# Performance work log

Measured on AMD Instinct MI355X. Metric: run time of the kernel, lower is better.

Reference implementation:

```python
import jax, jax.numpy as jnp
import numpy as np

OBS = jnp.array([0, 3, 6, 9, 12])
LO, HI = 0.001, 2.0

def gamma(x):
    return LO + (HI - LO) * jax.nn.sigmoid(x)

def full_chain_rhs(y, k):
    # y: (B,13) species, k: (B,19) rate constants
    A, B_, C, D, E, F, G, H, I, J, K_, L, M = [y[..., i] for i in range(13)]
    (kf1, kf2, kf3, kf4, kf5, kf6, kf7, kf8, kf9, kf10, kf11, kf12,
     kr1, kr3, kr5, kr7, kr9, kr11, kr12) = [k[..., i] for i in range(19)]
    dA = -kf1 * A + kr1 * B_
    dB = kf1 * A - kr1 * B_ - kf2 * B_
    dC = kf2 * B_ - kf3 * C + kr3 * D
    dD = kf3 * C - kr3 * D - kf4 * D
    dE = kf4 * D - kf5 * E + kr5 * F
    dF = kf5 * E - kr5 * F - kf6 * F
    dG = kf6 * F - kf7 * G + kr7 * H
    dH = kf7 * G - kr7 * H - kf8 * H
    dI = kf8 * H - kf9 * I + kr9 * J
    dJ = kf9 * I - kr9 * J - kf10 * J
    dK = kf10 * J - kf11 * K_ + kr11 * L
    dL = kf11 * K_ - kr11 * L - kf12 * L + kr12 * M
    dM = kf12 * L - kr12 * M
    return jnp.stack([dA, dB, dC, dD, dE, dF, dG, dH, dI, dJ, dK, dL, dM], axis=-1)

def rk4_step(y, dt, k):
    # y:(B,13) dt:(B,1) k:(B,19)
    k1 = full_chain_rhs(y, k)
    k2 = full_chain_rhs(y + 0.5 * dt * k1, k)
    k3 = full_chain_rhs(y + 0.5 * dt * k2, k)
    k4 = full_chain_rhs(y + dt * k3, k)
    return jnp.maximum(y + dt / 6.0 * (k1 + 2.0 * k2 + 2.0 * k3 + k4), 0.0)

def setup_inputs() -> dict:
    B, K, U, P = 2048, 256, 4, 5
    LIFT, HID = 32, 128
    key = jax.random.key(0)
    ks = jax.random.split(key, 9)
    in_dim = U + P
    def xavier(k, shape):
        lim = np.sqrt(6.0 / (shape[0] + shape[1])).astype(np.float32)
        return jax.random.uniform(k, shape, jnp.float32, -lim, lim)
    return {
        "y0": jax.random.uniform(ks[0], (B, P), jnp.float32),
        "u_seq": jax.random.normal(ks[1], (B, K, U), jnp.float32) * 0.1,
        "dt_seq": jax.random.uniform(ks[2], (B, K), jnp.float32, 0.01, 0.1),
        "y_seq": jax.random.uniform(ks[3], (B, K, P), jnp.float32),
        "W_lift": xavier(ks[4], (in_dim, LIFT)),
        "b_lift": jnp.zeros((LIFT,), jnp.float32),
        "w_ih": xavier(ks[5], (3 * HID, LIFT)),
        "w_hh": xavier(ks[6], (3 * HID, HID)),
        "b_ih": jnp.zeros((3 * HID,), jnp.float32),
        "b_hh": jnp.zeros((3 * HID,), jnp.float32),
        "W_head": xavier(ks[7], (HID, 19)),
        "b_head": jnp.zeros((19,), jnp.float32),
        "u_to_y_jump": jax.random.normal(ks[8], (U, P), jnp.float32) * 0.05,
        "tf_every": 50,
    }

def reference(y0, u_seq, dt_seq, y_seq, W_lift, b_lift, w_ih, w_hh, b_ih, b_hh, W_head, b_head, u_to_y_jump, tf_every):
    B, K, _ = u_seq.shape
    HID = w_hh.shape[1]
    # init hidden full state: 0.01 everywhere, obs slots get y0 + 0.01
    y_full0 = jnp.full((B, 13), 0.01, u_seq.dtype).at[:, OBS].set(y0 + 0.01)
    h0 = jnp.zeros((B, HID), u_seq.dtype)
    t = jnp.arange(K)
    tf_mask = (t > 0) & (t % tf_every == 0)  # teacher-forcing steps
    y_seq_prev = jnp.concatenate([jnp.zeros_like(y_seq[:, :1]), y_seq[:, :-1]], axis=1)
    xs = (jnp.swapaxes(u_seq, 0, 1), dt_seq.T[..., None],
          jnp.swapaxes(y_seq_prev, 0, 1), tf_mask)

    def step(carry, x):
        y_full, h = carry
        u_k, dt_k, y_prev_tf, m = x
        y_obs_prev = y_full[:, OBS]
        y_prev_in = jax.lax.stop_gradient(jnp.where(m, y_prev_tf, y_obs_prev))
        feat = jnp.concatenate([u_k, y_prev_in], axis=-1)
        lifted = jax.nn.silu(feat @ W_lift + b_lift)
        # PyTorch GRU cell
        gx = lifted @ w_ih.T + b_ih
        gh = h @ w_hh.T + b_hh
        rx, zx, nx = jnp.split(gx, 3, axis=-1)
        rh, zh, nh = jnp.split(gh, 3, axis=-1)
        r = jax.nn.sigmoid(rx + rh)
        z = jax.nn.sigmoid(zx + zh)
        n = jnp.tanh(nx + r * nh)
        h_new = (1.0 - z) * n + z * h
        theta = gamma(h_new @ W_head + b_head)  # (B,19), all bounds (0.001,2.0)
        y_obs_jump = y_obs_prev + u_k @ u_to_y_jump
        y_full_jump = y_full.at[:, OBS].set(y_obs_jump)
        y_full_next = rk4_step(y_full_jump, dt_k, theta)  # n_sub=1 as in forward
        return (y_full_next, h_new), (y_full_next[:, OBS], theta)

    _, (y_out, theta_out) = jax.lax.scan(step, (y_full0, h0), xs)
    return jnp.swapaxes(y_out, 0, 1), jnp.swapaxes(theta_out, 0, 1)
```

## Files before the change

kernel.cpp:

```cpp
#include <hip/hip_runtime.h>
#include <cstddef>
#include <cstdint>

#define NB 8
#define NTHREADS 640
#define HID 128
#define LIFT 32
#define NSP 13
#define NTH 19

typedef __attribute__((ext_vector_type(8))) short short8;
typedef __attribute__((ext_vector_type(4))) float f32x4;

__device__ const int c_kidx[13][4] = {
  {0,12,0,0},{0,12,1,0},{1,2,13,0},{2,13,3,0},{3,4,14,0},{4,14,5,0},
  {5,6,15,0},{6,15,7,0},{7,8,16,0},{8,16,9,0},{9,10,17,0},{10,17,11,18},{11,18,0,0}
};
__device__ const int c_yidx[13][4] = {
  {0,1,0,0},{0,1,1,0},{1,2,3,0},{2,3,3,0},{3,4,5,0},{4,5,5,0},
  {5,6,7,0},{6,7,7,0},{7,8,9,0},{8,9,9,0},{9,10,11,0},{10,11,11,12},{11,12,0,0}
};
__device__ const float c_sgn[13][4] = {
  {-1.f, 1.f, 0.f, 0.f},{ 1.f,-1.f,-1.f, 0.f},{ 1.f,-1.f, 1.f, 0.f},
  { 1.f,-1.f,-1.f, 0.f},{ 1.f,-1.f, 1.f, 0.f},{ 1.f,-1.f,-1.f, 0.f},
  { 1.f,-1.f, 1.f, 0.f},{ 1.f,-1.f,-1.f, 0.f},{ 1.f,-1.f, 1.f, 0.f},
  { 1.f,-1.f,-1.f, 0.f},{ 1.f,-1.f, 1.f, 0.f},{ 1.f,-1.f,-1.f, 1.f},
  { 1.f,-1.f, 0.f, 0.f}
};

__device__ __forceinline__ uint32_t pk(float a, float b) {
  uint32_t ua = __float_as_uint(a), ub = __float_as_uint(b);
  ua = (ua + 0x7FFFu + ((ua >> 16) & 1u)) >> 16;
  ub = (ub + 0x7FFFu + ((ub >> 16) & 1u)) >> 16;
  return ua | (ub << 16);
}
__device__ __forceinline__ float sigm(float a) { return 1.f/(1.f + __expf(-a)); }

union FragU { uint4 u; short8 s; };
__device__ __forceinline__ short8 ldfrag(const float* p) {
  FragU t;
  const float4 a = *reinterpret_cast<const float4*>(p);
  const float4 b = *reinterpret_cast<const float4*>(p+4);
  t.u = make_uint4(pk(a.x,a.y), pk(a.z,a.w), pk(b.x,b.y), pk(b.z,b.w));
  return t.s;
}

struct Smem {
  uint32_t whF[8*3*4*64*4];
  uint32_t whdF[2*4*64*4];
  uint32_t hF[4*64*4];
  uint32_t liftF[64*4];
  float theta[8*20];
};

__global__ __launch_bounds__(NTHREADS)
void fullmodel_rnn(const float* __restrict__ y0,
                   const float* __restrict__ u_seq,
                   const float* __restrict__ dt_seq,
                   const float* __restrict__ y_seq,
                   const float* __restrict__ W_lift,
                   const float* __restrict__ b_lift,
                   const float* __restrict__ w_ih,
                   const float* __restrict__ w_hh,
                   const float* __restrict__ b_ih,
                   const float* __restrict__ b_hh,
                   const float* __restrict__ W_head,
                   const float* __restrict__ b_head,
                   const float* __restrict__ u2y,
                   const int*  __restrict__ tf_every_p,
                   float* __restrict__ out,
                   int K, int theta_off)
{
  extern __shared__ __align__(16) char smem_raw[];
  Smem& S = *reinterpret_cast<Smem*>(smem_raw);

  const int tid  = threadIdx.x;
  const int wid  = tid >> 6;
  const int lane = tid & 63;
  const int q    = lane >> 4;
  const int col  = lane & 15;
  const int bg0  = blockIdx.x * NB;
  const int tf_every = tf_every_p[0];
  const bool gatew = (wid < 8);

  for (int f = tid; f < 8*3*4*64; f += NTHREADS) {
    int l = f & 63, idx = f >> 6;
    int s = idx & 3; idx >>= 2;
    int g = idx % 3, w = idx / 3;
    int row = 128*g + 16*w + (l & 15);
    int k0 = 32*s + 8*(l >> 4);
    const float* p = w_hh + (size_t)row*HID + k0;
    uint32_t* d = S.whF + (size_t)f*4;
    d[0]=pk(p[0],p[1]); d[1]=pk(p[2],p[3]); d[2]=pk(p[4],p[5]); d[3]=pk(p[6],p[7]);
  }
  for (int f = tid; f < 2*4*64; f += NTHREADS) {
    int l = f & 63, idx = f >> 6;
    int s = idx & 3, T = idx >> 2;
    int o = 16*T + (l & 15);
    int k0 = 32*s + 8*(l >> 4);
    uint32_t* d = S.whdF + (size_t)f*4;
    if (o < NTH) {
#pragma unroll
      for (int c=0;c<4;++c)
        d[c] = pk(W_head[(size_t)(k0+2*c)*NTH + o], W_head[(size_t)(k0+2*c+1)*NTH + o]);
    } else {
#pragma unroll
      for (int c=0;c<4;++c) d[c] = 0u;
    }
  }
  for (int f = tid; f < 4*64*4; f += NTHREADS) S.hF[f] = 0u;
  for (int f = tid; f < 64*4;   f += NTHREADS) S.liftF[f] = 0u;

  const uint32_t* hf_p  = &S.hF[lane*4];
  const uint32_t* lf_p  = &S.liftF[lane*4];
  const uint32_t* whp   = S.whF + ((size_t)wid*12*64 + lane)*4;
  const uint32_t* whdp  = S.whdF + (size_t)lane*4;

  float bsumR[4], bsumZ[4], bihn_[4], bhhn_[4], h_old[4];
  short8 wir, wiz, win;
  if (gatew) {
    const int rowR = 16*wid + col, kq = 8*q;
    wir = ldfrag(w_ih + (size_t)rowR*LIFT + kq);
    wiz = ldfrag(w_ih + (size_t)(128+rowR)*LIFT + kq);
    win = ldfrag(w_ih + (size_t)(256+rowR)*LIFT + kq);
#pragma unroll
    for (int r2=0;r2<4;++r2) {
      const int i0 = 16*wid + 4*q + r2;
      bsumR[r2] = b_ih[i0]     + b_hh[i0];
      bsumZ[r2] = b_ih[128+i0] + b_hh[128+i0];
      bihn_[r2] = b_ih[256+i0];
      bhhn_[r2] = b_hh[256+i0];
      h_old[r2] = 0.f;
    }
  }

  float bhd[2][4] = {{0,0,0,0},{0,0,0,0}};
  float wa0=0,wa1=0,wa2=0,wa3=0,wa4=0,wa5=0,wa6=0,wa7=0,wa8=0;
  float wb0=0,wb1=0,wb2=0,wb3=0,wb4=0,wb5=0,wb6=0,wb7=0,wb8=0;
  float blA=0.f, blB=0.f;
  const int base_b = (wid == 9) ? 4 : 0;
  const int b_loc = lane / NSP, rs = lane - NSP*b_loc;
  const bool rk_lane = (!gatew) && (lane < 52);
  const int bl8 = base_b + b_loc;
  const int gb = bg0 + (rk_lane ? bl8 : 0);
  const bool obs = rk_lane && (rs % 3 == 0);
  const int ro = rs / 3;
  float y_reg=0.f, u_cur=0.f, f_src=0.f;
  float sg_[4]={0,0,0,0}, u2yv[4]={0,0,0,0};
  int ksrc[4]={0,0,0,0}, ysrc[4]={0,0,0,0};
  float* outT0 = out; float* outY = out;
  if (!gatew) {
#pragma unroll
    for (int T=0;T<2;++T)
#pragma unroll
      for (int r2=0;r2<4;++r2) {
        const int o = 16*T + 4*q + r2;
        bhd[T][r2] = (o < NTH) ? b_head[o] : 0.f;
      }
    const int li = 2*col;
    wa0=W_lift[0*32+li]; wa1=W_lift[1*32+li]; wa2=W_lift[2*32+li];
    wa3=W_lift[3*32+li]; wa4=W_lift[4*32+li]; wa5=W_lift[5*32+li];
    wa6=W_lift[6*32+li]; wa7=W_lift[7*32+li]; wa8=W_lift[8*32+li];
    wb0=W_lift[0*32+li+1]; wb1=W_lift[1*32+li+1]; wb2=W_lift[2*32+li+1];
    wb3=W_lift[3*32+li+1]; wb4=W_lift[4*32+li+1]; wb5=W_lift[5*32+li+1];
    wb6=W_lift[6*32+li+1]; wb7=W_lift[7*32+li+1]; wb8=W_lift[8*32+li+1];
    blA = b_lift[li]; blB = b_lift[li+1];
    outT0 = out + (size_t)theta_off + ((size_t)(bg0+col))*K*NTH + 4*q;
    __builtin_amdgcn_s_setprio(2);
  }
  if (rk_lane) {
#pragma unroll
    for (int j=0;j<4;++j) { sg_[j]=c_sgn[rs][j]; ksrc[j]=c_kidx[rs][j]; ysrc[j]=NSP*b_loc + c_yidx[rs][j]; }
    y_reg = 0.01f + (obs ? y0[gb*5 + ro] : 0.f);
    if (rs < 4) u_cur = u_seq[(size_t)gb*K*4 + rs];
    if (obs) { for (int d=0;d<4;++d) u2yv[d] = u2y[d*5 + ro]; }
    f_src = y_reg;
    outY = out + ((size_t)gb*K)*5 + ro;
  }
  __syncthreads();

  for (int k = 0; k <= K; ++k) {
    f32x4 accR={0,0,0,0}, accZ={0,0,0,0}, accNH={0,0,0,0};

    if (gatew) {
      if (k < K) {
        FragU h0,h1,h2,h3;
        h0.u = *reinterpret_cast<const uint4*>(hf_p);
        h1.u = *reinterpret_cast<const uint4*>(hf_p + 256);
        h2.u = *reinterpret_cast<const uint4*>(hf_p + 512);
        h3.u = *reinterpret_cast<const uint4*>(hf_p + 768);
#pragma unroll
        for (int ss=0; ss<4; ++ss) {
          FragU ar,az,an;
          ar.u = *reinterpret_cast<const uint4*>(whp + (0*4+ss)*256);
          az.u = *reinterpret_cast<const uint4*>(whp + (1*4+ss)*256);
          an.u = *reinterpret_cast<const uint4*>(whp + (2*4+ss)*256);
          const short8 hb = (ss==0)?h0.s:(ss==1)?h1.s:(ss==2)?h2.s:h3.s;
          accR  = __builtin_amdgcn_mfma_f32_16x16x32_bf16(ar.s, hb, accR, 0,0,0);
          accZ  = __builtin_amdgcn_mfma_f32_16x16x32_bf16(az.s, hb, accZ, 0,0,0);
          accNH = __builtin_amdgcn_mfma_f32_16x16x32_bf16(an.s, hb, accNH, 0,0,0);
        }
      }
    } else {
      const int s = k - 1;
      float dt_v=0.f, u_nxt=0.f, ysq_v=0.f;
      if (rk_lane) {
        if (k >= 1) {
          if (rs == 4) dt_v  = dt_seq[(size_t)gb*K + s];
          if (obs)     ysq_v = y_seq[((size_t)gb*K + s)*5 + ro];
        }
        if (k < K && rs < 4) u_nxt = u_seq[((size_t)gb*K + k)*4 + rs];
      }
      if (k >= 1) {
        f32x4 at0={0,0,0,0}, at1={0,0,0,0};
        FragU h0,h1,h2,h3;
        h0.u = *reinterpret_cast<const uint4*>(hf_p);
        h1.u = *reinterpret_cast<const uint4*>(hf_p + 256);
        h2.u = *reinterpret_cast<const uint4*>(hf_p + 512);
        h3.u = *reinterpret_cast<const uint4*>(hf_p + 768);
#pragma unroll
        for (int ss=0; ss<4; ++ss) {
          FragU a0,a1;
          a0.u = *reinterpret_cast<const uint4*>(whdp + (0*4+ss)*256);
          a1.u = *reinterpret_cast<const uint4*>(whdp + (1*4+ss)*256);
          const short8 hb = (ss==0)?h0.s:(ss==1)?h1.s:(ss==2)?h2.s:h3.s;
          at0 = __builtin_amdgcn_mfma_f32_16x16x32_bf16(a0.s, hb, at0, 0,0,0);
          at1 = __builtin_amdgcn_mfma_f32_16x16x32_bf16(a1.s, hb, at1, 0,0,0);
        }
        if (col >= base_b && col < base_b + 4) {
          f32x4 th0;
#pragma unroll
          for (int r2=0;r2<4;++r2) th0[r2] = 0.001f + 1.999f*sigm(at0[r2] + bhd[0][r2]);
          *reinterpret_cast<f32x4*>(&S.theta[col*20 + 4*q]) = th0;
          outT0[0]=th0[0]; outT0[1]=th0[1]; outT0[2]=th0[2]; outT0[3]=th0[3];
          if (q == 0) {
            f32x4 th1;
#pragma unroll
            for (int r2=0;r2<4;++r2) th1[r2] = 0.001f + 1.999f*sigm(at1[r2] + bhd[1][r2]);
            *reinterpret_cast<f32x4*>(&S.theta[col*20 + 16]) = th1;
            outT0[16]=th1[0]; outT0[17]=th1[1]; outT0[18]=th1[2];
          }
        }
        if (rk_lane) {
          const float dtv = __shfl(dt_v, NSP*b_loc + 4);
          const float u0 = __shfl(u_cur, NSP*b_loc + 0);
          const float u1 = __shfl(u_cur, NSP*b_loc + 1);
          const float u2 = __shfl(u_cur, NSP*b_loc + 2);
          const float u3 = __shfl(u_cur, NSP*b_loc + 3);
          const float q0 = sg_[0]*S.theta[bl8*20 + ksrc[0]];
          const float q1 = sg_[1]*S.theta[bl8*20 + ksrc[1]];
          const float q2 = sg_[2]*S.theta[bl8*20 + ksrc[2]];
          const float q3 = sg_[3]*S.theta[bl8*20 + ksrc[3]];
          float yj = y_reg;
          if (obs) yj += u0*u2yv[0] + u1*u2yv[1] + u2*u2yv[2] + u3*u2yv[3];
          float yc = yj;
          const float k1 = q0*__shfl(yc,ysrc[0]) + q1*__shfl(yc,ysrc[1]) + q2*__shfl(yc,ysrc[2]) + q3*__shfl(yc,ysrc[3]);
          yc = fmaf(0.5f*dtv, k1, yj);
          const float k2 = q0*__shfl(yc,ysrc[0]) + q1*__shfl(yc,ysrc[1]) + q2*__shfl(yc,ysrc[2]) + q3*__shfl(yc,ysrc[3]);
          yc = fmaf(0.5f*dtv, k2, yj);
          const float k3 = q0*__shfl(yc,ysrc[0]) + q1*__shfl(yc,ysrc[1]) + q2*__shfl(yc,ysrc[2]) + q3*__shfl(yc,ysrc[3]);
          yc = fmaf(dtv, k3, yj);
          const float k4 = q0*__shfl(yc,ysrc[0]) + q1*__shfl(yc,ysrc[1]) + q2*__shfl(yc,ysrc[2]) + q3*__shfl(yc,ysrc[3]);
          const float yn = fmaxf(fmaf(dtv*(1.f/6.f), k1 + 2.f*k2 + 2.f*k3 + k4, yj), 0.f);
          y_reg = yn;
          if (obs) *outY = yn;
          if (k < K) {
            const bool m_next = (k % tf_every) == 0;
            u_cur = u_nxt;
            if (obs) f_src = m_next ? ysq_v : yn;
          }
        }
        outT0 += NTH; outY += 5;
      }
      if (k < K) {
        const int g4 = NSP*(lane >> 4);
        const float fu0 = __shfl(u_cur, g4+0), fu1 = __shfl(u_cur, g4+1);
        const float fu2 = __shfl(u_cur, g4+2), fu3 = __shfl(u_cur, g4+3);
        const float fy0 = __shfl(f_src, g4+0), fy1 = __shfl(f_src, g4+3);
        const float fy2 = __shfl(f_src, g4+6), fy3 = __shfl(f_src, g4+9);
        const float fy4 = __shfl(f_src, g4+12);
        float a = blA + fu0*wa0 + fu1*wa1 + fu2*wa2 + fu3*wa3
                      + fy0*wa4 + fy1*wa5 + fy2*wa6 + fy3*wa7 + fy4*wa8;
        float b = blB + fu0*wb0 + fu1*wb1 + fu2*wb2 + fu3*wb3
                      + fy0*wb4 + fy1*wb5 + fy2*wb6 + fy3*wb7 + fy4*wb8;
        const float va = a*sigm(a), vb = b*sigm(b);
        const int bL = base_b + (lane >> 4);
        S.liftF[(col>>2)*64 + bL*4 + (col&3)] = pk(va, vb);
      }
    }
    __syncthreads();

    if (gatew && k < K) {
      FragU lf; lf.u = *reinterpret_cast<const uint4*>(lf_p);
      accR = __builtin_amdgcn_mfma_f32_16x16x32_bf16(wir, lf.s, accR, 0,0,0);
      accZ = __builtin_amdgcn_mfma_f32_16x16x32_bf16(wiz, lf.s, accZ, 0,0,0);
      f32x4 z4 = {0,0,0,0};
      f32x4 accNX = __builtin_amdgcn_mfma_f32_16x16x32_bf16(win, lf.s, z4, 0,0,0);
      float hn[4];
#pragma unroll
      for (int r2=0;r2<4;++r2) {
        const float rg = sigm(accR[r2] + bsumR[r2]);
        const float zg = sigm(accZ[r2] + bsumZ[r2]);
        const float nx = accNX[r2] + bihn_[r2];
        const float nh = accNH[r2] + bhhn_[r2];
        const float e  = __expf(2.f*(nx + rg*nh));
        const float ng = 1.f - 2.f/(e + 1.f);
        hn[r2] = (1.f - zg)*ng + zg*h_old[r2];
        h_old[r2] = hn[r2];
      }
      const int word = (wid>>1)*256 + ((((2*wid)+(q>>1))&3)*16 + col)*4 + 2*(q&1);
      *reinterpret_cast<uint2*>(&S.hF[word]) = make_uint2(pk(hn[0],hn[1]), pk(hn[2],hn[3]));
    }
    __syncthreads();
  }
}

extern "C" void kernel_launch(void* const* d_in, const int* in_sizes, int n_in,
                              void* d_out, int out_size, void* d_ws, size_t ws_size,
                              hipStream_t stream) {
  const float* y0     = (const float*)d_in[0];
  const float* u_seq  = (const float*)d_in[1];
  const float* dt_seq = (const float*)d_in[2];
  const float* y_seq  = (const float*)d_in[3];
  const float* W_lift = (const float*)d_in[4];
  const float* b_lift = (const float*)d_in[5];
  const float* w_ih   = (const float*)d_in[6];
  const float* w_hh   = (const float*)d_in[7];
  const float* b_ih   = (const float*)d_in[8];
  const float* b_hh   = (const float*)d_in[9];
  const float* W_head = (const float*)d_in[10];
  const float* b_head = (const float*)d_in[11];
  const float* u2y    = (const float*)d_in[12];
  const int*   tfe    = (const int*)d_in[13];
  float* out = (float*)d_out;

  const int B = in_sizes[0] / 5;
  const int K = in_sizes[2] / B;
  const int theta_off = B * K * 5;

  (void)hipFuncSetAttribute((const void*)fullmodel_rnn,
                            hipFuncAttributeMaxDynamicSharedMemorySize,
                            (int)sizeof(Smem));

  dim3 grid(B / NB), block(NTHREADS);
  hipLaunchKernelGGL(fullmodel_rnn, grid, block, sizeof(Smem), stream,
                     y0, u_seq, dt_seq, y_seq, W_lift, b_lift, w_ih, w_hh,
                     b_ih, b_hh, W_head, b_head, u2y, tfe, out, K, theta_off);
}
```

Baseline: 677.6 us.

## Keep GRU recurrent weights in registers, simplify RK4 stencil, prefetch inputs

```diff
diff --git a/kernel.cpp b/kernel.cpp
--- a/kernel.cpp
+++ b/kernel.cpp
@@ -12,21 +12,13 @@
 typedef __attribute__((ext_vector_type(8))) short short8;
 typedef __attribute__((ext_vector_type(4))) float f32x4;
 
-__device__ const int c_kidx[13][4] = {
-  {0,12,0,0},{0,12,1,0},{1,2,13,0},{2,13,3,0},{3,4,14,0},{4,14,5,0},
-  {5,6,15,0},{6,15,7,0},{7,8,16,0},{8,16,9,0},{9,10,17,0},{10,17,11,18},{11,18,0,0}
-};
-__device__ const int c_yidx[13][4] = {
-  {0,1,0,0},{0,1,1,0},{1,2,3,0},{2,3,3,0},{3,4,5,0},{4,5,5,0},
-  {5,6,7,0},{6,7,7,0},{7,8,9,0},{8,9,9,0},{9,10,11,0},{10,11,11,12},{11,12,0,0}
-};
-__device__ const float c_sgn[13][4] = {
-  {-1.f, 1.f, 0.f, 0.f},{ 1.f,-1.f,-1.f, 0.f},{ 1.f,-1.f, 1.f, 0.f},
-  { 1.f,-1.f,-1.f, 0.f},{ 1.f,-1.f, 1.f, 0.f},{ 1.f,-1.f,-1.f, 0.f},
-  { 1.f,-1.f, 1.f, 0.f},{ 1.f,-1.f,-1.f, 0.f},{ 1.f,-1.f, 1.f, 0.f},
-  { 1.f,-1.f,-1.f, 0.f},{ 1.f,-1.f, 1.f, 0.f},{ 1.f,-1.f,-1.f, 1.f},
-  { 1.f,-1.f, 0.f, 0.f}
-};
+__device__ const int   c_kA [13] = {0,0,1,2,3,4,5,6,7,8,9,10,11};
+__device__ const int   c_kB1[13] = {0,12,2,13,4,14,6,15,8,16,10,17,18};
+__device__ const int   c_kB2[13] = {0,1,0,3,0,5,0,7,0,9,0,11,0};
+__device__ const int   c_kC [13] = {12,0,13,0,14,0,15,0,16,0,17,18,0};
+__device__ const float c_mA [13] = {0.f,1.f,1.f,1.f,1.f,1.f,1.f,1.f,1.f,1.f,1.f,1.f,1.f};
+__device__ const float c_mB2[13] = {0.f,1.f,0.f,1.f,0.f,1.f,0.f,1.f,0.f,1.f,0.f,1.f,0.f};
+__device__ const float c_mC [13] = {1.f,0.f,1.f,0.f,1.f,0.f,1.f,0.f,1.f,0.f,1.f,1.f,0.f};
 
 __device__ __forceinline__ uint32_t pk(float a, float b) {
   uint32_t ua = __float_as_uint(a), ub = __float_as_uint(b);
@@ -35,6 +27,20 @@
   return ua | (ub << 16);
 }
 __device__ __forceinline__ float sigm(float a) { return 1.f/(1.f + __expf(-a)); }
+
+__device__ __forceinline__ void sync_lds() {
+  __builtin_amdgcn_sched_barrier(0);
+  asm volatile("s_waitcnt lgkmcnt(0)" ::: "memory");
+  __builtin_amdgcn_s_barrier();
+  __builtin_amdgcn_sched_barrier(0);
+}
+
+__device__ __forceinline__ float rhs3(int am1, int ap1, float cA, float cB,
+                                      float cC, float yc) {
+  const float ym1 = __int_as_float(__builtin_amdgcn_ds_bpermute(am1, __float_as_int(yc)));
+  const float yp1 = __int_as_float(__builtin_amdgcn_ds_bpermute(ap1, __float_as_int(yc)));
+  return fmaf(cA, ym1, fmaf(cB, yc, cC * yp1));
+}
 
 union FragU { uint4 u; short8 s; };
 __device__ __forceinline__ short8 ldfrag(const float* p) {
@@ -46,14 +52,13 @@
 }
 
 struct Smem {
-  uint32_t whF[8*3*4*64*4];
   uint32_t whdF[2*4*64*4];
   uint32_t hF[4*64*4];
   uint32_t liftF[64*4];
   float theta[8*20];
 };
 
-__global__ __launch_bounds__(NTHREADS)
+__global__ __launch_bounds__(NTHREADS, 3)
 void fullmodel_rnn(const float* __restrict__ y0,
                    const float* __restrict__ u_seq,
                    const float* __restrict__ dt_seq,
@@ -83,16 +88,6 @@
   const int tf_every = tf_every_p[0];
   const bool gatew = (wid < 8);
 
-  for (int f = tid; f < 8*3*4*64; f += NTHREADS) {
-    int l = f & 63, idx = f >> 6;
-    int s = idx & 3; idx >>= 2;
-    int g = idx % 3, w = idx / 3;
-    int row = 128*g + 16*w + (l & 15);
-    int k0 = 32*s + 8*(l >> 4);
-    const float* p = w_hh + (size_t)row*HID + k0;
-    uint32_t* d = S.whF + (size_t)f*4;
-    d[0]=pk(p[0],p[1]); d[1]=pk(p[2],p[3]); d[2]=pk(p[4],p[5]); d[3]=pk(p[6],p[7]);
-  }
   for (int f = tid; f < 2*4*64; f += NTHREADS) {
     int l = f & 63, idx = f >> 6;
     int s = idx & 3, T = idx >> 2;
@@ -113,16 +108,22 @@
 
   const uint32_t* hf_p  = &S.hF[lane*4];
   const uint32_t* lf_p  = &S.liftF[lane*4];
-  const uint32_t* whp   = S.whF + ((size_t)wid*12*64 + lane)*4;
   const uint32_t* whdp  = S.whdF + (size_t)lane*4;
 
   float bsumR[4], bsumZ[4], bihn_[4], bhhn_[4], h_old[4];
-  short8 wir, wiz, win;
+  short8 wfR[4], wfZ[4], wfN[4], wir, wiz, win;
   if (gatew) {
     const int rowR = 16*wid + col, kq = 8*q;
     wir = ldfrag(w_ih + (size_t)rowR*LIFT + kq);
     wiz = ldfrag(w_ih + (size_t)(128+rowR)*LIFT + kq);
     win = ldfrag(w_ih + (size_t)(256+rowR)*LIFT + kq);
+    const float* wb = w_hh + (size_t)rowR*HID + kq;
+#pragma unroll
+    for (int ss=0; ss<4; ++ss) {
+      wfR[ss] = ldfrag(wb + 32*ss);
+      wfZ[ss] = ldfrag(wb + (size_t)128*HID + 32*ss);
+      wfN[ss] = ldfrag(wb + (size_t)256*HID + 32*ss);
+    }
 #pragma unroll
     for (int r2=0;r2<4;++r2) {
       const int i0 = 16*wid + 4*q + r2;
@@ -146,8 +147,11 @@
   const bool obs = rk_lane && (rs % 3 == 0);
   const int ro = rs / 3;
   float y_reg=0.f, u_cur=0.f, f_src=0.f;
-  float sg_[4]={0,0,0,0}, u2yv[4]={0,0,0,0};
-  int ksrc[4]={0,0,0,0}, ysrc[4]={0,0,0,0};
+  float u2yv[4]={0,0,0,0};
+  int kA_=0,kB1_=0,kB2_=0,kC_=0;
+  float mA_=0.f,mB2_=0.f,mC_=0.f;
+  int am1=0, ap1=0, tfc=1;
+  float dt_c=0.f, ysq_c=0.f, u_n=0.f;
   float* outT0 = out; float* outY = out;
   if (!gatew) {
 #pragma unroll
@@ -169,15 +173,17 @@
     __builtin_amdgcn_s_setprio(2);
   }
   if (rk_lane) {
-#pragma unroll
-    for (int j=0;j<4;++j) { sg_[j]=c_sgn[rs][j]; ksrc[j]=c_kidx[rs][j]; ysrc[j]=NSP*b_loc + c_yidx[rs][j]; }
+    kA_ = c_kA[rs]; kB1_ = c_kB1[rs]; kB2_ = c_kB2[rs]; kC_ = c_kC[rs];
+    mA_ = c_mA[rs]; mB2_ = c_mB2[rs]; mC_ = c_mC[rs];
+    am1 = 4 * ((lane > 0)  ? (lane - 1) : 0);
+    ap1 = 4 * ((lane < 51) ? (lane + 1) : 51);
     y_reg = 0.01f + (obs ? y0[gb*5 + ro] : 0.f);
     if (rs < 4) u_cur = u_seq[(size_t)gb*K*4 + rs];
     if (obs) { for (int d=0;d<4;++d) u2yv[d] = u2y[d*5 + ro]; }
     f_src = y_reg;
     outY = out + ((size_t)gb*K)*5 + ro;
   }
-  __syncthreads();
+  sync_lds();
 
   for (int k = 0; k <= K; ++k) {
     f32x4 accR={0,0,0,0}, accZ={0,0,0,0}, accNH={0,0,0,0};
@@ -191,25 +197,18 @@
         h3.u = *reinterpret_cast<const uint4*>(hf_p + 768);
 #pragma unroll
         for (int ss=0; ss<4; ++ss) {
-          FragU ar,az,an;
-          ar.u = *reinterpret_cast<const uint4*>(whp + (0*4+ss)*256);
-          az.u = *reinterpret_cast<const uint4*>(whp + (1*4+ss)*256);
-          an.u = *reinterpret_cast<const uint4*>(whp + (2*4+ss)*256);
           const short8 hb = (ss==0)?h0.s:(ss==1)?h1.s:(ss==2)?h2.s:h3.s;
-          accR  = __builtin_amdgcn_mfma_f32_16x16x32_bf16(ar.s, hb, accR, 0,0,0);
-          accZ  = __builtin_amdgcn_mfma_f32_16x16x32_bf16(az.s, hb, accZ, 0,0,0);
-          accNH = __builtin_amdgcn_mfma_f32_16x16x32_bf16(an.s, hb, accNH, 0,0,0);
+          accR  = __builtin_amdgcn_mfma_f32_16x16x32_bf16(wfR[ss], hb, accR, 0,0,0);
+          accZ  = __builtin_amdgcn_mfma_f32_16x16x32_bf16(wfZ[ss], hb, accZ, 0,0,0);
+          accNH = __builtin_amdgcn_mfma_f32_16x16x32_bf16(wfN[ss], hb, accNH, 0,0,0);
         }
       }
     } else {
-      const int s = k - 1;
-      float dt_v=0.f, u_nxt=0.f, ysq_v=0.f;
-      if (rk_lane) {
-        if (k >= 1) {
-          if (rs == 4) dt_v  = dt_seq[(size_t)gb*K + s];
-          if (obs)     ysq_v = y_seq[((size_t)gb*K + s)*5 + ro];
-        }
-        if (k < K && rs < 4) u_nxt = u_seq[((size_t)gb*K + k)*4 + rs];
+      float dt_p=0.f, ysq_p=0.f, u_p=0.f;
+      if (rk_lane && k < K) {
+        if (rs == 4)              dt_p  = dt_seq[(size_t)gb*K + k];
+        if (obs)                  ysq_p = y_seq[((size_t)gb*K + k)*5 + ro];
+        if (rs < 4 && (k+1) < K)  u_p   = u_seq[((size_t)gb*K + (k+1))*4 + rs];
       }
       if (k >= 1) {
         f32x4 at0={0,0,0,0}, at1={0,0,0,0};
@@ -242,32 +241,33 @@
           }
         }
         if (rk_lane) {
-          const float dtv = __shfl(dt_v, NSP*b_loc + 4);
+          const float dtv = __shfl(dt_c, NSP*b_loc + 4);
           const float u0 = __shfl(u_cur, NSP*b_loc + 0);
           const float u1 = __shfl(u_cur, NSP*b_loc + 1);
           const float u2 = __shfl(u_cur, NSP*b_loc + 2);
           const float u3 = __shfl(u_cur, NSP*b_loc + 3);
-          const float q0 = sg_[0]*S.theta[bl8*20 + ksrc[0]];
-          const float q1 = sg_[1]*S.theta[bl8*20 + ksrc[1]];
-          const float q2 = sg_[2]*S.theta[bl8*20 + ksrc[2]];
-          const float q3 = sg_[3]*S.theta[bl8*20 + ksrc[3]];
+          const float* thp = S.theta + bl8*20;
+          const float cA = mA_ * thp[kA_];
+          const float cB = -(thp[kB1_] + mB2_ * thp[kB2_]);
+          const float cC = mC_ * thp[kC_];
           float yj = y_reg;
           if (obs) yj += u0*u2yv[0] + u1*u2yv[1] + u2*u2yv[2] + u3*u2yv[3];
           float yc = yj;
-          const float k1 = q0*__shfl(yc,ysrc[0]) + q1*__shfl(yc,ysrc[1]) + q2*__shfl(yc,ysrc[2]) + q3*__shfl(yc,ysrc[3]);
+          const float k1 = rhs3(am1, ap1, cA, cB, cC, yc);
           yc = fmaf(0.5f*dtv, k1, yj);
-          const float k2 = q0*__shfl(yc,ysrc[0]) + q1*__shfl(yc,ysrc[1]) + q2*__shfl(yc,ysrc[2]) + q3*__shfl(yc,ysrc[3]);
+          const float k2 = rhs3(am1, ap1, cA, cB, cC, yc);
           yc = fmaf(0.5f*dtv, k2, yj);
-          const float k3 = q0*__shfl(yc,ysrc[0]) + q1*__shfl(yc,ysrc[1]) + q2*__shfl(yc,ysrc[2]) + q3*__shfl(yc,ysrc[3]);
+          const float k3 = rhs3(am1, ap1, cA, cB, cC, yc);
           yc = fmaf(dtv, k3, yj);
-          const float k4 = q0*__shfl(yc,ysrc[0]) + q1*__shfl(yc,ysrc[1]) + q2*__shfl(yc,ysrc[2]) + q3*__shfl(yc,ysrc[3]);
+          const float k4 = rhs3(am1, ap1, cA, cB, cC, yc);
           const float yn = fmaxf(fmaf(dtv*(1.f/6.f), k1 + 2.f*k2 + 2.f*k3 + k4, yj), 0.f);
           y_reg = yn;
           if (obs) *outY = yn;
           if (k < K) {
-            const bool m_next = (k % tf_every) == 0;
-            u_cur = u_nxt;
-            if (obs) f_src = m_next ? ysq_v : yn;
+            const bool m_next = (tfc == tf_every);
+            tfc = m_next ? 1 : (tfc + 1);
+            u_cur = u_n;
+            if (obs) f_src = m_next ? ysq_c : yn;
           }
         }
         outT0 += NTH; outY += 5;
@@ -287,8 +287,9 @@
         const int bL = base_b + (lane >> 4);
         S.liftF[(col>>2)*64 + bL*4 + (col&3)] = pk(va, vb);
       }
-    }
-    __syncthreads();
+      dt_c = dt_p; ysq_c = ysq_p; u_n = u_p;
+    }
+    sync_lds();
 
     if (gatew && k < K) {
       FragU lf; lf.u = *reinterpret_cast<const uint4*>(lf_p);
@@ -311,7 +312,7 @@
       const int word = (wid>>1)*256 + ((((2*wid)+(q>>1))&3)*16 + col)*4 + 2*(q&1);
       *reinterpret_cast<uint2*>(&S.hF[word]) = make_uint2(pk(hn[0],hn[1]), pk(hn[2],hn[3]));
     }
-    __syncthreads();
+    sync_lds();
   }
 }
 
```

Result: slower. 767.1 us (+13.2%).
